# Optimization experiments

Hardware: AMD Instinct MI355X
Metric: run time of the kernel (lower is better)

The kernel has to match this reference:

```python
import jax, jax.numpy as jnp
import numpy as np

N_QUBITS = 12
LAYERS = 2
BATCH = 1024


def _apply_1q(state, gate, q):
    # state: [B] + [2]*n (wire 0 = leading qubit axis); gate: [2,2] or [B,2,2]
    axis = 1 + q
    st = jnp.moveaxis(state, axis, -1)
    if gate.ndim == 2:
        st = jnp.einsum('ij,...j->...i', gate, st)
    else:  # batched gate (angle depends on the input sample)
        st = jnp.einsum('bij,b...j->b...i', gate, st)
    return jnp.moveaxis(st, -1, axis)


def _apply_cnot(state, c, t):
    # flip target axis on the control=1 slice
    ca, ta = 1 + c, 1 + t
    a0 = jnp.take(state, 0, axis=ca)
    a1 = jnp.take(state, 1, axis=ca)
    ta2 = ta - 1 if ta > ca else ta
    a1 = jnp.flip(a1, axis=ta2)
    return jnp.stack([a0, a1], axis=ca)


def _rx(a):
    # a: [B] -> gate [B,2,2]
    h = 0.5 * a
    c = jnp.cos(h).astype(jnp.complex64)
    s = (-1j) * jnp.sin(h).astype(jnp.complex64)
    return jnp.stack([jnp.stack([c, s], -1), jnp.stack([s, c], -1)], -2)


def _ry(a):
    h = 0.5 * a
    c = jnp.cos(h).astype(jnp.complex64)
    s = jnp.sin(h).astype(jnp.complex64)
    return jnp.stack([jnp.stack([c, -s], -1), jnp.stack([s, c], -1)], -2)


def _rz(a):
    h = 0.5 * a
    e0 = jnp.exp(-1j * h.astype(jnp.complex64))
    e1 = jnp.exp(1j * h.astype(jnp.complex64))
    z = jnp.zeros_like(e0)
    return jnp.stack([jnp.stack([e0, z], -1), jnp.stack([z, e1], -1)], -2)


def setup_inputs() -> dict:
    key = jax.random.key(0)
    k1, k2 = jax.random.split(key)
    x = jax.random.normal(k1, (BATCH, N_QUBITS), dtype=jnp.float32)
    theta = jax.random.normal(k2, (LAYERS, N_QUBITS, 2), dtype=jnp.float32)
    lam = jnp.ones((LAYERS, N_QUBITS), dtype=jnp.float32)
    return {"x": x, "theta": theta, "lam": lam}


def reference(x, theta, lam):
    B = x.shape[0]
    n = N_QUBITS
    # |0...0> state, batched: [B] + [2]*n
    state = jnp.zeros((B,) + (2,) * n, dtype=jnp.complex64)
    state = state.at[(slice(None),) + (0,) * n].set(1.0)
    for l in range(LAYERS):
        for q in range(n):
            state = _apply_1q(state, _rx(lam[l, q] * x[:, q]), q)
        for q in range(n):
            state = _apply_cnot(state, q, (q + 1) % n)
        for q in range(n):
            state = _apply_1q(state, _ry(theta[l, q, 0]), q)
            state = _apply_1q(state, _rz(theta[l, q, 1]), q)
    probs = state.real ** 2 + state.imag ** 2  # [B] + [2]*n
    zs = []
    for q in range(n):
        axes = tuple(i for i in range(1, n + 1) if i != 1 + q)
        p = jnp.sum(probs, axis=axes)  # [B, 2]
        zs.append(p[:, 0] - p[:, 1])   # <Z_q>
    return jnp.stack(zs, axis=1)  # [B, n_qubits]
```

## Files before the change

kernel.cpp:

```cpp
#include <hip/hip_runtime.h>
#include <math.h>

#define NQ 12
#define TPB 256


__device__ __forceinline__ float rfl(float x) {
    return __int_as_float(__builtin_amdgcn_readfirstlane(__float_as_int(x)));
}

__device__ __forceinline__ float2 pk_mul(float2 a, float2 b) {
    float2 d;
    asm("v_pk_mul_f32 %0, %1, %2" : "=v"(d) : "v"(a), "v"(b));
    return d;
}
__device__ __forceinline__ float2 pk_fma(float2 a, float2 b, float2 c) {
    float2 d;
    asm("v_pk_fma_f32 %0, %1, %2, %3" : "=v"(d) : "v"(a), "v"(b), "v"(c));
    return d;
}

#define FOR_PAIRS4(RB, STMT) do {                                     \
    const int msk_ = 1 << (RB);                                       \
    _Pragma("unroll")                                                 \
    for (int h_ = 0; h_ < 8; ++h_) {                                  \
        const int i0 = ((h_ & ~(msk_ - 1)) << 1) | (h_ & (msk_ - 1)); \
        const int i1 = i0 | msk_;                                     \
        STMT;                                                         \
    } } while (0)

#define ADDR_A(r) (VA ^ (257 * (r)))
#define ADDR_B(r) (VB ^ (17 * (r)))
#define ADDR_C(r) (VC ^ (r))

#define LOCAL_X(AS, AD) do {                                          \
    _Pragma("unroll")                                                 \
    for (int r_ = 0; r_ < 16; ++r_) S[AS(r_)] = v[r_];                \
    _Pragma("unroll")                                                 \
    for (int r_ = 0; r_ < 16; ++r_) v[r_] = S[AD(r_)];                \
  } while (0)

#define M_GATE(q, RB) do {                                                  \
        float4 A4v = mA[q]; float2 P2v = mB[q];                             \
        float az = rfl(A4v.z), aw = rfl(A4v.w);                             \
        float px = rfl(P2v.x), py = rfl(P2v.y);                             \
        float cth = rfl(A4v.x), sth = rfl(A4v.y);                           \
        float2 c2  = make_float2(cth, cth);                                 \
        float2 s2  = make_float2(sth, sth);                                 \
        float2 ms2 = make_float2(-sth, -sth);                               \
        FOR_PAIRS4(RB, {                                                    \
            float2 a1 = v[i1];                                              \
            float2 b1 = make_float2(az*a1.x - aw*a1.y,                      \
                                    az*a1.y + aw*a1.x);                     \
            float2 n0 = pk_fma(b1, ms2, pk_mul(v[i0], c2));                 \
            float2 n1 = pk_fma(v[i0], s2, pk_mul(b1, c2));                  \
            v[i0] = n0;                                                     \
            v[i1] = make_float2(px*n1.x - py*n1.y,                          \
                                px*n1.y + py*n1.x);                         \
        });                                                                 \
    } while (0)

#define RY_GATE(q, RB) do {                                                 \
        float2 csv = coY[q];                                                \
        float cth = rfl(csv.x), sth = rfl(csv.y);                           \
        float2 c2  = make_float2(cth, cth);                                 \
        float2 s2  = make_float2(sth, sth);                                 \
        float2 ms2 = make_float2(-sth, -sth);                               \
        FOR_PAIRS4(RB, {                                                    \
            float2 n0 = pk_fma(v[i1], ms2, pk_mul(v[i0], c2));              \
            float2 n1 = pk_fma(v[i0], s2, pk_mul(v[i1], c2));               \
            v[i0] = n0; v[i1] = n1;                                         \
        });                                                                 \
    } while (0)

#define M_PHASE(QB)  do { _Pragma("unroll")                                 \
    for (int d_ = 0; d_ < 4; ++d_) M_GATE((QB) + d_, 3 - d_); } while (0)
#define RY_PHASE(QB) do { _Pragma("unroll")                                 \
    for (int d_ = 0; d_ < 4; ++d_) RY_GATE((QB) + d_, 3 - d_); } while (0)

__global__ __launch_bounds__(TPB) void vqc_kernel(
    const float* __restrict__ x,
    const float* __restrict__ th,
    const float* __restrict__ lm,
    float* __restrict__ out)
{
    __shared__ float2 S[4096];
    __shared__ float4 mA[12];
    __shared__ float2 mB[12];
    __shared__ float2 coI[12];
    __shared__ float2 coY[12];
    __shared__ float red[4 * 12];

    const int b = blockIdx.x;
    const int t = threadIdx.x;
    const int l = t & 63;
    const int w = t >> 6;

    const int kC = (t ^ (t >> 4)) & 15;
    const int VA = (t & 0xF0) | kC;
    const int VB = ((t >> 4) << 8) | kC;
    const int VC = (t << 4) | kC;
    int Ft;
    {
        int yt = t ^ (t >> 1); yt ^= yt >> 2; yt ^= yt >> 4; yt ^= yt >> 8;
        int pt = (yt & 0x7FF) | ((__popc(t) & 1) << 11);
        Ft = (pt & ~15) | ((pt ^ (pt >> 4) ^ (pt >> 8)) & 15);
    }

    if (t < 12) {
        float h = 0.5f * lm[t] * x[b * NQ + t];
        float c, s; __sincosf(h, &s, &c);
        coI[t] = make_float2(c, s);
    } else if (t < 24) {
        int q = t - 12;
        float h = 0.5f * th[24 + 2 * q];
        float c, s; __sincosf(h, &s, &c);
        coY[q] = make_float2(c, s);
    } else if (t < 36) {
        int q = t - 24;
        float ha = 0.5f * lm[12 + q] * x[b * NQ + q];
        float hy = 0.5f * th[2 * q];
        float hz = 0.5f * th[2 * q + 1];
        float ca, sa, cy, sy, cz, sz;
        __sincosf(ha, &sa, &ca);
        __sincosf(hy, &sy, &cy);
        __sincosf(hz, &sz, &cz);
        float ax = ca*cy*cz + sa*sy*sz;
        float ay = -(ca*cy*sz + sa*sy*cz);
        float bx = ca*sy*cz - sa*cy*sz;
        float by = ca*sy*sz - sa*cy*cz;
        float na = ax*ax + ay*ay, nb = bx*bx + by*by;
        float ra = rsqrtf(fmaxf(na, 1e-30f));
        float rb = rsqrtf(fmaxf(nb, 1e-30f));
        float ux = ax*ra, uy = ay*ra;
        float wx = bx*rb, wy = by*rb;
        mA[q] = make_float4(na*ra, nb*rb,
                            ux*wx - uy*wy, -(ux*wy + uy*wx));
        mB[q] = make_float2(ux*wx + uy*wy, ux*wy - uy*wx);
    }
    __syncthreads();

    float2 v[16];

    {
        const int g = (t ^ (t >> 1)) & 0x3F;
        float Pt = 1.0f;
#pragma unroll
        for (int m = 0; m < 6; ++m) {
            float2 cs = coI[7 - m];
            Pt *= ((g >> m) & 1) ? cs.y : cs.x;
        }
        const int ct = __popc(g);
        const int t0 = t & 1, t7 = (t >> 7) & 1;
        const int e1 = ((t >> 6) ^ (t >> 7)) & 1;
        float2 q11 = coI[11], q10 = coI[10], q9 = coI[9],
               q8 = coI[8], q1 = coI[1], q0 = coI[0];
        const float u8  = t0 ? q8.y : q8.x;
        const float u8n = t0 ? q8.x : q8.y;
        const float u1  = e1 ? q1.y : q1.x;
        const float u1n = e1 ? q1.x : q1.y;
        const float u0  = t7 ? q0.y : q0.x;
        const float u0n = t7 ? q0.x : q0.y;
#pragma unroll
        for (int r = 0; r < 16; ++r) {
            const int r0 = r & 1, r1 = (r >> 1) & 1, r2 = (r >> 2) & 1,
                      r3 = (r >> 3) & 1;
            const int b11 = r0 ^ r1, b10 = r1 ^ r2, b9 = r2 ^ r3;
            float m = Pt * (b11 ? q11.y : q11.x) * (b10 ? q10.y : q10.x)
                         * (b9 ? q9.y : q9.x) * (r3 ? u8n : u8)
                         * (r0 ? u1n : u1) * (r0 ? u0n : u0);
            int k = (ct + b11 + b10 + b9 + (r3 ^ t0) + (r0 ^ e1) + (r0 ^ t7)) & 3;
            v[r].x = (k == 0) ? m : ((k == 2) ? -m : 0.0f);
            v[r].y = (k == 3) ? m : ((k == 1) ? -m : 0.0f);
        }
    }

    M_PHASE(8);
    LOCAL_X(ADDR_C, ADDR_B);
    M_PHASE(4);
#pragma unroll
    for (int r = 0; r < 16; ++r) S[ADDR_B(r)] = v[r];
    __syncthreads();
#pragma unroll
    for (int r = 0; r < 16; ++r) v[r] = S[ADDR_A(r)];
    M_PHASE(0);

    __syncthreads();
#pragma unroll
    for (int r = 0; r < 16; ++r) {
        const int jr = r << 8;
        int yr = jr ^ (jr >> 1); yr ^= yr >> 2; yr ^= yr >> 4; yr ^= yr >> 8;
        const int pr = (yr & 0x7FF) | (((__popc(jr) ^ (jr >> 11)) & 1) << 11);
        const int Gr = (pr & ~15) | ((pr ^ (pr >> 4) ^ (pr >> 8)) & 15);
        S[Ft ^ Gr] = v[r];
    }
    __syncthreads();
#pragma unroll
    for (int r = 0; r < 16; ++r) v[r] = S[ADDR_A(r)];

    RY_PHASE(0);
    __syncthreads();
#pragma unroll
    for (int r = 0; r < 16; ++r) S[ADDR_A(r)] = v[r];
    __syncthreads();
#pragma unroll
    for (int r = 0; r < 16; ++r) v[r] = S[ADDR_B(r)];
    RY_PHASE(4);
    LOCAL_X(ADDR_B, ADDR_C);
    RY_PHASE(8);

    float vals[5] = {0.f, 0.f, 0.f, 0.f, 0.f};
#pragma unroll
    for (int r = 0; r < 16; ++r) {
        float p = fmaf(v[r].x, v[r].x, v[r].y * v[r].y);
        vals[0] += p;
        vals[1] += (r & 8) ? -p : p;
        vals[2] += (r & 4) ? -p : p;
        vals[3] += (r & 2) ? -p : p;
        vals[4] += (r & 1) ? -p : p;
    }
#pragma unroll
    for (int k = 0; k < 6; ++k) {
        const float sgn = ((l >> k) & 1) ? -1.f : 1.f;
#pragma unroll
        for (int m = 0; m < 5; ++m) {
            float tmp = __shfl_xor(vals[m], 1 << k, 64);
            vals[m] = fmaf(sgn, vals[m], tmp);
        }
    }
    if (l == 0) {
        red[w * 12 + 0]  = vals[0];
        red[w * 12 + 8]  = vals[1];
        red[w * 12 + 9]  = vals[2];
        red[w * 12 + 10] = vals[3];
        red[w * 12 + 11] = vals[4];
    } else if (__popc(l) == 1) {
        int q = 8 - __ffs(l);
        red[w * 12 + q] = vals[0];
    }
    __syncthreads();
    if (t < NQ) {
        float acc = 0.f;
#pragma unroll
        for (int ww = 0; ww < 4; ++ww) {
            if (t < 2) {
                float pv = red[ww * 12 + 0];
                acc += ((ww >> (1 - t)) & 1) ? -pv : pv;
            } else {
                acc += red[ww * 12 + t];
            }
        }
        out[b * NQ + t] = acc;
    }
}

extern "C" void kernel_launch(void* const* d_in, const int* in_sizes, int n_in,
                              void* d_out, int out_size, void* d_ws, size_t ws_size,
                              hipStream_t stream) {
    const int B = in_sizes[0] / NQ;
    vqc_kernel<<<B, TPB, 0, stream>>>((const float*)d_in[0],
                                      (const float*)d_in[1],
                                      (const float*)d_in[2],
                                      (float*)d_out);
}
```

Baseline: 75.46 us.

## Apply fused gate as packed complex 2x2 matmul and restructure final reduction

Measured after the change: 73.29 us. 1.03x faster.

```diff
diff --git a/kernel.cpp b/kernel.cpp
--- a/kernel.cpp
+++ b/kernel.cpp
@@ -5,10 +5,6 @@
 #define TPB 256
 
 
-__device__ __forceinline__ float rfl(float x) {
-    return __int_as_float(__builtin_amdgcn_readfirstlane(__float_as_int(x)));
-}
-
 __device__ __forceinline__ float2 pk_mul(float2 a, float2 b) {
     float2 d;
     asm("v_pk_mul_f32 %0, %1, %2" : "=v"(d) : "v"(a), "v"(b));
@@ -19,14 +15,33 @@
     asm("v_pk_fma_f32 %0, %1, %2, %3" : "=v"(d) : "v"(a), "v"(b), "v"(c));
     return d;
 }
-
-#define FOR_PAIRS4(RB, STMT) do {                                     \
+__device__ __forceinline__ float2 pk_fma_sw0(float2 a, float2 b, float2 c) {
+    float2 d;
+    asm("v_pk_fma_f32 %0, %1, %2, %3 op_sel:[1,0,0] op_sel_hi:[0,1,1]"
+        : "=v"(d) : "v"(a), "v"(b), "v"(c));
+    return d;
+}
+__device__ __forceinline__ float2 pk_fma_n1(float2 a, float2 b, float2 c) {
+    float2 d;
+    asm("v_pk_fma_f32 %0, %1, %2, %3 neg_lo:[0,1,0] neg_hi:[0,1,0]"
+        : "=v"(d) : "v"(a), "v"(b), "v"(c));
+    return d;
+}
+__device__ __forceinline__ float2 pk_fma_sw0n1(float2 a, float2 b, float2 c) {
+    float2 d;
+    asm("v_pk_fma_f32 %0, %1, %2, %3 op_sel:[1,0,0] op_sel_hi:[0,1,1] "
+        "neg_lo:[0,1,0] neg_hi:[0,1,0]"
+        : "=v"(d) : "v"(a), "v"(b), "v"(c));
+    return d;
+}
+
+#define FOR_PAIRS4(RB, ...) do {                                      \
     const int msk_ = 1 << (RB);                                       \
     _Pragma("unroll")                                                 \
     for (int h_ = 0; h_ < 8; ++h_) {                                  \
         const int i0 = ((h_ & ~(msk_ - 1)) << 1) | (h_ & (msk_ - 1)); \
         const int i1 = i0 | msk_;                                     \
-        STMT;                                                         \
+        __VA_ARGS__;                                                  \
     } } while (0)
 
 #define ADDR_A(r) (VA ^ (257 * (r)))
@@ -41,36 +56,33 @@
   } while (0)
 
 #define M_GATE(q, RB) do {                                                  \
-        float4 A4v = mA[q]; float2 P2v = mB[q];                             \
-        float az = rfl(A4v.z), aw = rfl(A4v.w);                             \
-        float px = rfl(P2v.x), py = rfl(P2v.y);                             \
-        float cth = rfl(A4v.x), sth = rfl(A4v.y);                           \
-        float2 c2  = make_float2(cth, cth);                                 \
-        float2 s2  = make_float2(sth, sth);                                 \
-        float2 ms2 = make_float2(-sth, -sth);                               \
-        FOR_PAIRS4(RB, {                                                    \
-            float2 a1 = v[i1];                                              \
-            float2 b1 = make_float2(az*a1.x - aw*a1.y,                      \
-                                    az*a1.y + aw*a1.x);                     \
-            float2 n0 = pk_fma(b1, ms2, pk_mul(v[i0], c2));                 \
-            float2 n1 = pk_fma(v[i0], s2, pk_mul(b1, c2));                  \
-            v[i0] = n0;                                                     \
-            v[i1] = make_float2(px*n1.x - py*n1.y,                          \
-                                px*n1.y + py*n1.x);                         \
-        });                                                                 \
+        const float2 ar = gm[q][0];                                         \
+        const float2 ai = gm[q][1];                                         \
+        const float2 br = gm[q][2];                                         \
+        const float2 bi = gm[q][3];                                         \
+        FOR_PAIRS4(RB,                                                      \
+            const float2 v0 = v[i0];                                        \
+            const float2 v1 = v[i1];                                        \
+            float2 n0 = pk_mul(v0, ar);                                     \
+            n0 = pk_fma_sw0(v0, ai, n0);                                    \
+            n0 = pk_fma_n1(v1, br, n0);                                     \
+            n0 = pk_fma_sw0(v1, bi, n0);                                    \
+            float2 n1 = pk_mul(v0, br);                                     \
+            n1 = pk_fma_sw0(v0, bi, n1);                                    \
+            n1 = pk_fma(v1, ar, n1);                                        \
+            n1 = pk_fma_sw0n1(v1, ai, n1);                                  \
+            v[i0] = n0; v[i1] = n1;                                         \
+        );                                                                  \
     } while (0)
 
 #define RY_GATE(q, RB) do {                                                 \
-        float2 csv = coY[q];                                                \
-        float cth = rfl(csv.x), sth = rfl(csv.y);                           \
-        float2 c2  = make_float2(cth, cth);                                 \
-        float2 s2  = make_float2(sth, sth);                                 \
-        float2 ms2 = make_float2(-sth, -sth);                               \
-        FOR_PAIRS4(RB, {                                                    \
-            float2 n0 = pk_fma(v[i1], ms2, pk_mul(v[i0], c2));              \
+        const float2 c2 = gy[q][0];                                         \
+        const float2 s2 = gy[q][1];                                         \
+        FOR_PAIRS4(RB,                                                      \
+            float2 n0 = pk_fma_n1(v[i1], s2, pk_mul(v[i0], c2));            \
             float2 n1 = pk_fma(v[i0], s2, pk_mul(v[i1], c2));               \
             v[i0] = n0; v[i1] = n1;                                         \
-        });                                                                 \
+        );                                                                  \
     } while (0)
 
 #define M_PHASE(QB)  do { _Pragma("unroll")                                 \
@@ -78,17 +90,16 @@
 #define RY_PHASE(QB) do { _Pragma("unroll")                                 \
     for (int d_ = 0; d_ < 4; ++d_) RY_GATE((QB) + d_, 3 - d_); } while (0)
 
-__global__ __launch_bounds__(TPB) void vqc_kernel(
+__global__ __launch_bounds__(TPB, 4) void vqc_kernel(
     const float* __restrict__ x,
     const float* __restrict__ th,
     const float* __restrict__ lm,
     float* __restrict__ out)
 {
     __shared__ float2 S[4096];
-    __shared__ float4 mA[12];
-    __shared__ float2 mB[12];
+    __shared__ float2 gm[12][4];
+    __shared__ float2 gy[12][2];
     __shared__ float2 coI[12];
-    __shared__ float2 coY[12];
     __shared__ float red[4 * 12];
 
     const int b = blockIdx.x;
@@ -115,7 +126,8 @@
         int q = t - 12;
         float h = 0.5f * th[24 + 2 * q];
         float c, s; __sincosf(h, &s, &c);
-        coY[q] = make_float2(c, s);
+        gy[q][0] = make_float2(c, c);
+        gy[q][1] = make_float2(s, s);
     } else if (t < 36) {
         int q = t - 24;
         float ha = 0.5f * lm[12 + q] * x[b * NQ + q];
@@ -129,14 +141,10 @@
         float ay = -(ca*cy*sz + sa*sy*cz);
         float bx = ca*sy*cz - sa*cy*sz;
         float by = ca*sy*sz - sa*cy*cz;
-        float na = ax*ax + ay*ay, nb = bx*bx + by*by;
-        float ra = rsqrtf(fmaxf(na, 1e-30f));
-        float rb = rsqrtf(fmaxf(nb, 1e-30f));
-        float ux = ax*ra, uy = ay*ra;
-        float wx = bx*rb, wy = by*rb;
-        mA[q] = make_float4(na*ra, nb*rb,
-                            ux*wx - uy*wy, -(ux*wy + uy*wx));
-        mB[q] = make_float2(ux*wx + uy*wy, ux*wy - uy*wx);
+        gm[q][0] = make_float2(ax, ax);
+        gm[q][1] = make_float2(-ay, ay);
+        gm[q][2] = make_float2(bx, bx);
+        gm[q][3] = make_float2(-by, by);
     }
     __syncthreads();
 
@@ -199,7 +207,6 @@
     for (int r = 0; r < 16; ++r) v[r] = S[ADDR_A(r)];
 
     RY_PHASE(0);
-    __syncthreads();
 #pragma unroll
     for (int r = 0; r < 16; ++r) S[ADDR_A(r)] = v[r];
     __syncthreads();
@@ -209,16 +216,34 @@
     LOCAL_X(ADDR_B, ADDR_C);
     RY_PHASE(8);
 
-    float vals[5] = {0.f, 0.f, 0.f, 0.f, 0.f};
-#pragma unroll
-    for (int r = 0; r < 16; ++r) {
-        float p = fmaf(v[r].x, v[r].x, v[r].y * v[r].y);
-        vals[0] += p;
-        vals[1] += (r & 8) ? -p : p;
-        vals[2] += (r & 4) ? -p : p;
-        vals[3] += (r & 2) ? -p : p;
-        vals[4] += (r & 1) ? -p : p;
-    }
+    float p[16];
+#pragma unroll
+    for (int r = 0; r < 16; ++r)
+        p[r] = fmaf(v[r].x, v[r].x, v[r].y * v[r].y);
+    float sA[8], dA[8];
+#pragma unroll
+    for (int k = 0; k < 8; ++k) {
+        sA[k] = p[2 * k] + p[2 * k + 1];
+        dA[k] = p[2 * k] - p[2 * k + 1];
+    }
+    float z11 = ((dA[0] + dA[1]) + (dA[2] + dA[3]))
+              + ((dA[4] + dA[5]) + (dA[6] + dA[7]));
+    float sC[4], dC[4];
+#pragma unroll
+    for (int k = 0; k < 4; ++k) {
+        sC[k] = sA[2 * k] + sA[2 * k + 1];
+        dC[k] = sA[2 * k] - sA[2 * k + 1];
+    }
+    float z10 = (dC[0] + dC[1]) + (dC[2] + dC[3]);
+    float e0 = sC[0] + sC[1], f0 = sC[0] - sC[1];
+    float e1s = sC[2] + sC[3], f1 = sC[2] - sC[3];
+    float vals[5];
+    vals[0] = e0 + e1s;
+    vals[1] = e0 - e1s;
+    vals[2] = f0 + f1;
+    vals[3] = z10;
+    vals[4] = z11;
+
 #pragma unroll
     for (int k = 0; k < 6; ++k) {
         const float sgn = ((l >> k) & 1) ? -1.f : 1.f;
```
